# Kernel tuning notes

Hardware: AMD Instinct MI355X
Metric: run time of the kernel (lower is better)

## Reference

```python
import jax, jax.numpy as jnp
import numpy as np

NUM_QUERIES = 300

def setup_inputs() -> dict:
    key = jax.random.key(0)
    k1, k2, k3, k4 = jax.random.split(key, 4)
    B, A, L, H = 32, 8400, 80, 256
    return {
        "enc_outputs_class": jax.random.normal(k1, (B, A, L), dtype=jnp.float32),
        "enc_outputs_coord_logits_plus_anchors": jax.random.normal(k2, (B, A, 4), dtype=jnp.float32),
        "output_memory": jax.random.normal(k3, (B, A, H), dtype=jnp.float32),
        "sources_last_element": jax.random.normal(k4, (B, H, 20, 20), dtype=jnp.float32),
    }

def reference(enc_outputs_class, enc_outputs_coord_logits_plus_anchors, output_memory, sources_last_element):
    # enc_outputs_class: [B, A, L]; reduce class dim, top-k over anchors A.
    cls_max = jnp.max(enc_outputs_class, axis=-1)                      # [B, A]
    _, topk_ind = jax.lax.top_k(cls_max, NUM_QUERIES)                  # [B, Q], sorted desc
    idx = topk_ind[:, :, None]                                         # [B, Q, 1]

    def gather(data):  # per-batch gather along anchor axis
        return jnp.take_along_axis(data, idx, axis=1)

    reference_points_unact = gather(enc_outputs_coord_logits_plus_anchors)  # [B, Q, 4]
    enc_topk_logits = gather(enc_outputs_class)                             # [B, Q, L]
    enc_topk_bboxes = jax.nn.sigmoid(reference_points_unact)               # [B, Q, 4]

    # learn_initial_query=False: target comes from gathered encoder memory (stop-grad)
    target = jax.lax.stop_gradient(gather(output_memory))                   # [B, Q, H]
    init_reference_points = jax.lax.stop_gradient(reference_points_unact)  # [B, Q, 4]
    return (init_reference_points, target, enc_topk_logits, enc_topk_bboxes)
```

## Files before the change

### kernel.cpp

```cpp
#include <hip/hip_runtime.h>
#include <stdint.h>

#define BATCH 32
#define NA    8400
#define NL    80
#define NH    256
#define NK    300
#define NBIN  8192

#define OUT0 0
#define OUT1 38400
#define OUT2 2496000
#define OUT3 3264000

__device__ __forceinline__ unsigned mapf(float f) {
    unsigned u = __float_as_uint(f);
    return (u & 0x80000000u) ? ~u : (u | 0x80000000u);
}

__global__ __launch_bounds__(256) void cls_max_kernel(const float* __restrict__ cls,
                                                      unsigned* __restrict__ out_u) {
    int tid = threadIdx.x;
    int row = blockIdx.x * 64 + (tid >> 2);
    int sub = tid & 3;
    if (row >= BATCH * NA) return;
    const float4* p = (const float4*)(cls + (size_t)row * NL);
    float m = -3.4e38f;
#pragma unroll
    for (int q = 0; q < 5; ++q) {
        float4 v = p[sub + q * 4];
        m = fmaxf(m, fmaxf(fmaxf(v.x, v.y), fmaxf(v.z, v.w)));
    }
    m = fmaxf(m, __shfl_xor(m, 1));
    m = fmaxf(m, __shfl_xor(m, 2));
    if (sub == 0) out_u[row] = mapf(m);
}

__global__ __launch_bounds__(1024) void topk_kernel(const unsigned* __restrict__ u_in,
                                                    int* __restrict__ topk_idx) {
    __shared__ unsigned hist[NBIN];
    __shared__ unsigned long long keys[1024];
    __shared__ unsigned wsum[16], wsuf[16];
    __shared__ unsigned s_thr, s_count;

    int tid  = threadIdx.x;
    int lane = tid & 63;
    int wid  = tid >> 6;
    int b    = blockIdx.x;
    const unsigned* ub = u_in + b * NA;

    for (int i = tid; i < NBIN; i += 1024) hist[i] = 0;
    if (tid == 0) s_count = 0;
    __syncthreads();

    for (int i = tid; i < NA; i += 1024) atomicAdd(&hist[ub[i] >> 19], 1u);
    __syncthreads();

    unsigned base = tid * 8;
    unsigned L = 0;
#pragma unroll
    for (int j = 0; j < 8; ++j) L += hist[base + j];
    unsigned s = L;
#pragma unroll
    for (int off = 1; off < 64; off <<= 1) {
        unsigned t = __shfl_down(s, off);
        if (lane + off < 64) s += t;
    }
    if (lane == 0) wsum[wid] = s;
    __syncthreads();
    if (tid == 0) {
        unsigned acc = 0;
        for (int w = 15; w >= 0; --w) { acc += wsum[w]; wsuf[w] = acc; }
    }
    __syncthreads();
    unsigned above = (wid < 15 ? wsuf[wid + 1] : 0u) + (s - L);
    unsigned acc = above;
#pragma unroll
    for (int j = 7; j >= 0; --j) {
        unsigned S = acc + hist[base + j];
        if (S >= (unsigned)NK && acc < (unsigned)NK) s_thr = base + (unsigned)j;
        acc = S;
    }
    __syncthreads();

    unsigned T = s_thr;
    for (int i = tid; i < NA; i += 1024) {
        unsigned v = ub[i];
        if ((v >> 19) >= T) {
            unsigned pos = atomicAdd(&s_count, 1u);
            if (pos < 1024) keys[pos] = ((unsigned long long)(~v) << 32) | (unsigned)i;
        }
    }
    __syncthreads();

    unsigned count = s_count < 1024u ? s_count : 1024u;
    if (tid < (int)count) {
        unsigned long long mykey = keys[tid];
        int rank = 0;
        for (unsigned j = 0; j < count; ++j) rank += (keys[j] < mykey);
        if (rank < NK) topk_idx[b * NK + rank] = (int)(mykey & 0xFFFFFFFFull);
    }
}

__global__ __launch_bounds__(256) void gather_kernel(const float* __restrict__ cls,
                                                     const float* __restrict__ coord,
                                                     const float* __restrict__ mem,
                                                     const int* __restrict__ topk_idx,
                                                     float* __restrict__ out) {
    int wid  = blockIdx.x * 4 + (threadIdx.x >> 6);
    int lane = threadIdx.x & 63;
    if (wid >= BATCH * NK) return;
    int b = wid / NK;
    int q = wid - b * NK;
    int idx = topk_idx[b * NK + q];
    size_t srow = (size_t)b * NA + (size_t)idx;
    size_t drow = (size_t)b * NK + (size_t)q;

    const float4* msrc = (const float4*)(mem + srow * NH);
    float4*       mdst = (float4*)(out + OUT1 + drow * NH);
    mdst[lane] = msrc[lane];

    if (lane < 20) {
        const float4* lsrc = (const float4*)(cls + srow * NL);
        float4*       ldst = (float4*)(out + OUT2 + drow * NL);
        ldst[lane] = lsrc[lane];
    }

    if (lane == 0) {
        float4 c = ((const float4*)(coord + srow * 4))[0];
        ((float4*)(out + OUT0 + drow * 4))[0] = c;
        float4 s;
        s.x = 1.0f / (1.0f + __expf(-c.x));
        s.y = 1.0f / (1.0f + __expf(-c.y));
        s.z = 1.0f / (1.0f + __expf(-c.z));
        s.w = 1.0f / (1.0f + __expf(-c.w));
        ((float4*)(out + OUT3 + drow * 4))[0] = s;
    }
}

extern "C" void kernel_launch(void* const* d_in, const int* in_sizes, int n_in,
                              void* d_out, int out_size, void* d_ws, size_t ws_size,
                              hipStream_t stream) {
    const float* cls   = (const float*)d_in[0];
    const float* coord = (const float*)d_in[1];
    const float* mem   = (const float*)d_in[2];

    unsigned* ws_u = (unsigned*)d_ws;
    int*      topk = (int*)((char*)d_ws + (size_t)BATCH * NA * 4);
    float*    out  = (float*)d_out;

    cls_max_kernel<<<(BATCH * NA) / 64, 256, 0, stream>>>(cls, ws_u);
    topk_kernel<<<BATCH, 1024, 0, stream>>>(ws_u, topk);
    gather_kernel<<<(BATCH * NK) / 4, 256, 0, stream>>>(cls, coord, mem, topk, out);
}
```

Measured before the change: 38.73 us.

## Build per-batch radix histogram in cls_max kernel via global atomics

The per-batch histogram of the top 13 bits of each mapped max is now built inside the class-max kernel with global atomics, so the single-block-per-batch top-k kernel no longer zeroes and fills a shared histogram. That kernel just loads its 8 bins per thread from global memory. A small zeroing kernel is added, which costs an extra launch and adds global atomic contention on hot bins (values cluster near similar maxima). The serial select kernel with only 32 blocks gets shorter in exchange.

Measured after the change: 94.01 us. +142.8%, slower.

```diff
diff --git a/kernel.cpp b/kernel.cpp
--- a/kernel.cpp
+++ b/kernel.cpp
@@ -13,13 +13,22 @@
 #define OUT2 2496000
 #define OUT3 3264000
 
+#define WS_U_OFF    0
+#define WS_TOPK_OFF 1075200
+#define WS_HIST_OFF 1113600
+
 __device__ __forceinline__ unsigned mapf(float f) {
     unsigned u = __float_as_uint(f);
     return (u & 0x80000000u) ? ~u : (u | 0x80000000u);
 }
 
+__global__ __launch_bounds__(256) void zero_hist_kernel(uint4* __restrict__ p) {
+    p[blockIdx.x * 256 + threadIdx.x] = make_uint4(0u, 0u, 0u, 0u);
+}
+
 __global__ __launch_bounds__(256) void cls_max_kernel(const float* __restrict__ cls,
-                                                      unsigned* __restrict__ out_u) {
+                                                      unsigned* __restrict__ out_u,
+                                                      unsigned* __restrict__ hist_g) {
     int tid = threadIdx.x;
     int row = blockIdx.x * 64 + (tid >> 2);
     int sub = tid & 3;
@@ -33,12 +42,17 @@
     }
     m = fmaxf(m, __shfl_xor(m, 1));
     m = fmaxf(m, __shfl_xor(m, 2));
-    if (sub == 0) out_u[row] = mapf(m);
+    if (sub == 0) {
+        unsigned u = mapf(m);
+        out_u[row] = u;
+        int b = row / NA;
+        atomicAdd(&hist_g[b * NBIN + (u >> 19)], 1u);
+    }
 }
 
-__global__ __launch_bounds__(1024) void topk_kernel(const unsigned* __restrict__ u_in,
-                                                    int* __restrict__ topk_idx) {
-    __shared__ unsigned hist[NBIN];
+__global__ __launch_bounds__(1024) void select_kernel(const unsigned* __restrict__ u_in,
+                                                      const unsigned* __restrict__ hist_g,
+                                                      int* __restrict__ topk_idx) {
     __shared__ unsigned long long keys[1024];
     __shared__ unsigned wsum[16], wsuf[16];
     __shared__ unsigned s_thr, s_count;
@@ -49,17 +63,15 @@
     int b    = blockIdx.x;
     const unsigned* ub = u_in + b * NA;
 
-    for (int i = tid; i < NBIN; i += 1024) hist[i] = 0;
     if (tid == 0) s_count = 0;
-    __syncthreads();
 
-    for (int i = tid; i < NA; i += 1024) atomicAdd(&hist[ub[i] >> 19], 1u);
-    __syncthreads();
-
-    unsigned base = tid * 8;
+    const uint4* h4 = (const uint4*)(hist_g + b * NBIN + tid * 8);
+    uint4 a0 = h4[0], a1 = h4[1];
+    unsigned h[8] = {a0.x, a0.y, a0.z, a0.w, a1.x, a1.y, a1.z, a1.w};
     unsigned L = 0;
 #pragma unroll
-    for (int j = 0; j < 8; ++j) L += hist[base + j];
+    for (int j = 0; j < 8; ++j) L += h[j];
+
     unsigned s = L;
 #pragma unroll
     for (int off = 1; off < 64; off <<= 1) {
@@ -77,8 +89,8 @@
     unsigned acc = above;
 #pragma unroll
     for (int j = 7; j >= 0; --j) {
-        unsigned S = acc + hist[base + j];
-        if (S >= (unsigned)NK && acc < (unsigned)NK) s_thr = base + (unsigned)j;
+        unsigned S = acc + h[j];
+        if (S >= (unsigned)NK && acc < (unsigned)NK) s_thr = (unsigned)(tid * 8 + j);
         acc = S;
     }
     __syncthreads();
@@ -145,11 +157,13 @@
     const float* coord = (const float*)d_in[1];
     const float* mem   = (const float*)d_in[2];
 
-    unsigned* ws_u = (unsigned*)d_ws;
-    int*      topk = (int*)((char*)d_ws + (size_t)BATCH * NA * 4);
+    unsigned* ws_u = (unsigned*)((char*)d_ws + WS_U_OFF);
+    int*      topk = (int*)((char*)d_ws + WS_TOPK_OFF);
+    unsigned* hist = (unsigned*)((char*)d_ws + WS_HIST_OFF);
     float*    out  = (float*)d_out;
 
-    cls_max_kernel<<<(BATCH * NA) / 64, 256, 0, stream>>>(cls, ws_u);
-    topk_kernel<<<BATCH, 1024, 0, stream>>>(ws_u, topk);
+    zero_hist_kernel<<<BATCH * NBIN * 4 / 4096, 256, 0, stream>>>((uint4*)hist);
+    cls_max_kernel<<<(BATCH * NA) / 64, 256, 0, stream>>>(cls, ws_u, hist);
+    select_kernel<<<BATCH, 1024, 0, stream>>>(ws_u, hist, topk);
     gather_kernel<<<(BATCH * NK) / 4, 256, 0, stream>>>(cls, coord, mem, topk, out);
 }
```

## Fuse top-k selection with gather, replicating selection across 8 blocks per batch

Applied to the files above, without the earlier changes.

Merges the top-k kernel and the gather kernel into one launch. Each batch gets 8 blocks; every block redundantly recomputes the histogram threshold and ranking, keeps the sorted indices in shared memory, and then gathers its strided share of the 300 rows. Anchor values are also held in registers so the second pass does not reload them from global memory. This removes one kernel launch and the round trip of indices through global memory, at the cost of doing the selection work eight times over.

Measured after the change: 34.73 us. 10.3% less time.

```diff
diff --git a/kernel.cpp b/kernel.cpp
--- a/kernel.cpp
+++ b/kernel.cpp
@@ -36,30 +36,49 @@
     if (sub == 0) out_u[row] = mapf(m);
 }
 
-__global__ __launch_bounds__(1024) void topk_kernel(const unsigned* __restrict__ u_in,
-                                                    int* __restrict__ topk_idx) {
+__global__ __launch_bounds__(1024) void select_gather_kernel(
+        const unsigned* __restrict__ u_in,
+        const float*    __restrict__ cls,
+        const float*    __restrict__ coord,
+        const float*    __restrict__ mem,
+        float*          __restrict__ out) {
     __shared__ unsigned hist[NBIN];
     __shared__ unsigned long long keys[1024];
+    __shared__ int ord[NK];
     __shared__ unsigned wsum[16], wsuf[16];
     __shared__ unsigned s_thr, s_count;
 
     int tid  = threadIdx.x;
     int lane = tid & 63;
     int wid  = tid >> 6;
-    int b    = blockIdx.x;
+    int b    = blockIdx.x >> 3;
+    int sub  = blockIdx.x & 7;
     const unsigned* ub = u_in + b * NA;
 
     for (int i = tid; i < NBIN; i += 1024) hist[i] = 0;
     if (tid == 0) s_count = 0;
     __syncthreads();
 
-    for (int i = tid; i < NA; i += 1024) atomicAdd(&hist[ub[i] >> 19], 1u);
+    unsigned v[9];
+#pragma unroll
+    for (int k = 0; k < 9; ++k) {
+        int i = tid + k * 1024;
+        v[k] = (i < NA) ? ub[i] : 0u;
+    }
+#pragma unroll
+    for (int k = 0; k < 9; ++k) {
+        int i = tid + k * 1024;
+        if (i < NA) atomicAdd(&hist[v[k] >> 19], 1u);
+    }
     __syncthreads();
 
     unsigned base = tid * 8;
+    unsigned h[8];
+#pragma unroll
+    for (int j = 0; j < 8; ++j) h[j] = hist[base + j];
     unsigned L = 0;
 #pragma unroll
-    for (int j = 0; j < 8; ++j) L += hist[base + j];
+    for (int j = 0; j < 8; ++j) L += h[j];
     unsigned s = L;
 #pragma unroll
     for (int off = 1; off < 64; off <<= 1) {
@@ -77,18 +96,19 @@
     unsigned acc = above;
 #pragma unroll
     for (int j = 7; j >= 0; --j) {
-        unsigned S = acc + hist[base + j];
+        unsigned S = acc + h[j];
         if (S >= (unsigned)NK && acc < (unsigned)NK) s_thr = base + (unsigned)j;
         acc = S;
     }
     __syncthreads();
 
     unsigned T = s_thr;
-    for (int i = tid; i < NA; i += 1024) {
-        unsigned v = ub[i];
-        if ((v >> 19) >= T) {
+#pragma unroll
+    for (int k = 0; k < 9; ++k) {
+        int i = tid + k * 1024;
+        if (i < NA && (v[k] >> 19) >= T) {
             unsigned pos = atomicAdd(&s_count, 1u);
-            if (pos < 1024) keys[pos] = ((unsigned long long)(~v) << 32) | (unsigned)i;
+            if (pos < 1024) keys[pos] = ((unsigned long long)(~v[k]) << 32) | (unsigned)i;
         }
     }
     __syncthreads();
@@ -98,43 +118,34 @@
         unsigned long long mykey = keys[tid];
         int rank = 0;
         for (unsigned j = 0; j < count; ++j) rank += (keys[j] < mykey);
-        if (rank < NK) topk_idx[b * NK + rank] = (int)(mykey & 0xFFFFFFFFull);
+        if (rank < NK) ord[rank] = (int)(mykey & 0xFFFFFFFFull);
     }
-}
+    __syncthreads();
 
-__global__ __launch_bounds__(256) void gather_kernel(const float* __restrict__ cls,
-                                                     const float* __restrict__ coord,
-                                                     const float* __restrict__ mem,
-                                                     const int* __restrict__ topk_idx,
-                                                     float* __restrict__ out) {
-    int wid  = blockIdx.x * 4 + (threadIdx.x >> 6);
-    int lane = threadIdx.x & 63;
-    if (wid >= BATCH * NK) return;
-    int b = wid / NK;
-    int q = wid - b * NK;
-    int idx = topk_idx[b * NK + q];
-    size_t srow = (size_t)b * NA + (size_t)idx;
-    size_t drow = (size_t)b * NK + (size_t)q;
+    for (int q = sub + 8 * wid; q < NK; q += 8 * 16) {
+        int idx = ord[q];
+        size_t srow = (size_t)b * NA + (size_t)idx;
+        size_t drow = (size_t)b * NK + (size_t)q;
 
-    const float4* msrc = (const float4*)(mem + srow * NH);
-    float4*       mdst = (float4*)(out + OUT1 + drow * NH);
-    mdst[lane] = msrc[lane];
+        const float4* msrc = (const float4*)(mem + srow * NH);
+        float4*       mdst = (float4*)(out + OUT1 + drow * NH);
+        mdst[lane] = msrc[lane];
 
-    if (lane < 20) {
-        const float4* lsrc = (const float4*)(cls + srow * NL);
-        float4*       ldst = (float4*)(out + OUT2 + drow * NL);
-        ldst[lane] = lsrc[lane];
-    }
-
-    if (lane == 0) {
-        float4 c = ((const float4*)(coord + srow * 4))[0];
-        ((float4*)(out + OUT0 + drow * 4))[0] = c;
-        float4 s;
-        s.x = 1.0f / (1.0f + __expf(-c.x));
-        s.y = 1.0f / (1.0f + __expf(-c.y));
-        s.z = 1.0f / (1.0f + __expf(-c.z));
-        s.w = 1.0f / (1.0f + __expf(-c.w));
-        ((float4*)(out + OUT3 + drow * 4))[0] = s;
+        if (lane < 20) {
+            const float4* lsrc = (const float4*)(cls + srow * NL);
+            float4*       ldst = (float4*)(out + OUT2 + drow * NL);
+            ldst[lane] = lsrc[lane];
+        }
+        if (lane == 0) {
+            float4 c = ((const float4*)(coord + srow * 4))[0];
+            ((float4*)(out + OUT0 + drow * 4))[0] = c;
+            float4 sg;
+            sg.x = 1.0f / (1.0f + __expf(-c.x));
+            sg.y = 1.0f / (1.0f + __expf(-c.y));
+            sg.z = 1.0f / (1.0f + __expf(-c.z));
+            sg.w = 1.0f / (1.0f + __expf(-c.w));
+            ((float4*)(out + OUT3 + drow * 4))[0] = sg;
+        }
     }
 }
 
@@ -146,10 +157,8 @@
     const float* mem   = (const float*)d_in[2];
 
     unsigned* ws_u = (unsigned*)d_ws;
-    int*      topk = (int*)((char*)d_ws + (size_t)BATCH * NA * 4);
     float*    out  = (float*)d_out;
 
     cls_max_kernel<<<(BATCH * NA) / 64, 256, 0, stream>>>(cls, ws_u);
-    topk_kernel<<<BATCH, 1024, 0, stream>>>(ws_u, topk);
-    gather_kernel<<<(BATCH * NK) / 4, 256, 0, stream>>>(cls, coord, mem, topk, out);
+    select_gather_kernel<<<BATCH * 8, 1024, 0, stream>>>(ws_u, cls, coord, mem, out);
 }
```
